# Kernel tuning notes

Measured on AMD Instinct MI355X. Metric: run time of the kernel, lower is better.

## Reference

```python
import jax, jax.numpy as jnp
import numpy as np

NEG_SLOPE = 0.2   # PyG GATConv leaky_relu default
BN_EPS = 1e-5


def setup_inputs() -> dict:
    key = jax.random.key(0)
    ks = jax.random.split(key, 6)
    B, C, N, T = 8, 128, 64, 512   # batch, in_channels, electrodes, time_steps
    H, D = 4, 32                   # heads, per-head dim; OUT = H*D = 128
    E = 256                        # knn edges (k=4 per electrode)
    OUT = H * D
    x = jax.random.normal(ks[0], (B, C, N, T), dtype=jnp.float32)
    W = jax.random.normal(ks[1], (C, H, D), dtype=jnp.float32) / np.float32(np.sqrt(C))
    att_src = jax.random.normal(ks[2], (H, D), dtype=jnp.float32) / np.float32(np.sqrt(D))
    att_dst = jax.random.normal(ks[3], (H, D), dtype=jnp.float32) / np.float32(np.sqrt(D))
    bias = jnp.zeros((OUT,), dtype=jnp.float32)
    bn_gamma = jnp.ones((OUT,), jnp.float32)
    bn_beta = jnp.zeros((OUT,), jnp.float32)
    bn_mean = jnp.zeros((OUT,), jnp.float32)   # BatchNorm running stats (eval mode)
    bn_var = jnp.ones((OUT,), jnp.float32)
    edge_index = jax.random.randint(ks[4], (2, E), 0, N, dtype=jnp.int32)
    return dict(x=x, W=W, att_src=att_src, att_dst=att_dst, bias=bias,
                bn_gamma=bn_gamma, bn_beta=bn_beta, bn_mean=bn_mean,
                bn_var=bn_var, edge_index=edge_index)


def _gat(x, W, att_src, att_dst, bias, edge_index):
    # x: [BT, N, C]; fixed graph shared across all BT slices -> fully batched
    BT, N, C = x.shape
    H, D = att_src.shape
    loops = jnp.arange(N, dtype=edge_index.dtype)
    src = jnp.concatenate([edge_index[0], loops])   # GATConv add_self_loops=True
    dst = jnp.concatenate([edge_index[1], loops])   # [E']
    h = jnp.einsum('bnc,chd->bnhd', x, W)           # [BT,N,H,D]
    a_src = jnp.einsum('bnhd,hd->bnh', h, att_src)  # [BT,N,H]
    a_dst = jnp.einsum('bnhd,hd->bnh', h, att_dst)
    scores = jax.nn.leaky_relu(a_src[:, src] + a_dst[:, dst], NEG_SLOPE)  # [BT,E',H]
    scores_e = jnp.transpose(scores, (1, 0, 2))                           # [E',BT,H]
    # segment softmax over incoming edges of each target node
    m = jax.ops.segment_max(scores_e, dst, num_segments=N)               # [N,BT,H]
    ex = jnp.exp(scores_e - m[dst])
    denom = jax.ops.segment_sum(ex, dst, num_segments=N)
    alpha = ex / denom[dst]                                               # [E',BT,H]
    msgs = alpha[..., None] * jnp.transpose(h[:, src], (1, 0, 2, 3))      # [E',BT,H,D]
    agg = jax.ops.segment_sum(msgs, dst, num_segments=N)                  # [N,BT,H,D]
    out = jnp.transpose(agg, (1, 0, 2, 3)).reshape(BT, N, H * D) + bias   # concat heads
    return out


def reference(x, W, att_src, att_dst, bias, bn_gamma, bn_beta, bn_mean, bn_var, edge_index):
    B, C, N, T = x.shape
    xt = jnp.transpose(x, (0, 3, 2, 1)).reshape(B * T, N, C)  # loop dim batched
    g = _gat(xt, W, att_src, att_dst, bias, edge_index)        # [BT,N,OUT]
    g = g.mean(axis=1)                                         # mean over nodes -> [BT,OUT]
    OUT = g.shape[-1]
    g = g.reshape(B, T, OUT).transpose(0, 2, 1)                # [B,OUT,T]
    y = (g - bn_mean[:, None]) * jax.lax.rsqrt(bn_var[:, None] + BN_EPS) \
        * bn_gamma[:, None] + bn_beta[:, None]                 # BatchNorm1d (eval)
    return y[:, :, None, :]                                    # [B,OUT,1,T]
```

## Files before the change

kernel.cpp:

```cpp
#include <hip/hip_runtime.h>
#include <math.h>

#define B_ 8
#define C_ 128
#define N_ 64
#define T_ 512
#define H_ 4
#define D_ 32
#define OUT_ 128
#define E_ 256
#define EP_ 320
#define NEG_SLOPE 0.2f
#define BN_EPS 1e-5f
#define TC 8

__global__ void setup_kernel(const float* __restrict__ W,
                             const float* __restrict__ att_src,
                             const float* __restrict__ att_dst,
                             const int* __restrict__ edge_index,
                             float* __restrict__ wa,
                             int* __restrict__ iOff_g, int* __restrict__ iSrc_g,
                             int* __restrict__ oOff_g, int* __restrict__ oDst_g) {
  __shared__ int icnt[N_], ibase[N_ + 1], ifill[N_];
  __shared__ int ocnt[N_], obase[N_ + 1], ofill[N_];
  __shared__ int esrc[EP_], edst[EP_];
  int tid = threadIdx.x;

  for (int idx = tid; idx < C_ * 8; idx += blockDim.x) {
    int c = idx >> 3, j = idx & 7, h = j & 3;
    const float* att = (j < 4) ? att_src : att_dst;
    float s = 0.f;
    for (int d = 0; d < D_; ++d)
      s += W[(c * H_ + h) * D_ + d] * att[h * D_ + d];
    wa[idx] = s;
  }
  if (tid < N_) { icnt[tid] = 0; ifill[tid] = 0; ocnt[tid] = 0; ofill[tid] = 0; }
  __syncthreads();
  for (int e = tid; e < EP_; e += blockDim.x) {
    int s, d;
    if (e < E_) { s = edge_index[e]; d = edge_index[E_ + e]; }
    else        { s = e - E_;        d = e - E_; }
    esrc[e] = s; edst[e] = d;
    atomicAdd(&icnt[d], 1);
    atomicAdd(&ocnt[s], 1);
  }
  __syncthreads();
  if (tid == 0) {
    int ai = 0, ao = 0;
    for (int n = 0; n < N_; ++n) {
      ibase[n] = ai; ai += icnt[n];
      obase[n] = ao; ao += ocnt[n];
    }
    ibase[N_] = ai; obase[N_] = ao;
  }
  __syncthreads();
  if (tid <= N_) { iOff_g[tid] = ibase[tid]; oOff_g[tid] = obase[tid]; }
  for (int e = tid; e < EP_; e += blockDim.x) {
    int s = esrc[e], d = edst[e];
    int pi = ibase[d] + atomicAdd(&ifill[d], 1);
    iSrc_g[pi] = s;
    int po = obase[s] + atomicAdd(&ofill[s], 1);
    oDst_g[po] = d;
  }
}

#define P1FMA(J, WS) \
  acc[J].x = fmaf(xv[u].x, WS, acc[J].x); \
  acc[J].y = fmaf(xv[u].y, WS, acc[J].y); \
  acc[J].z = fmaf(xv[u].z, WS, acc[J].z); \
  acc[J].w = fmaf(xv[u].w, WS, acc[J].w);

__global__ __launch_bounds__(256, 2)
void mega_kernel(const float* __restrict__ x,
                 const float* __restrict__ wa_g,
                 const float* __restrict__ W,
                 const int* __restrict__ iOff_g, const int* __restrict__ iSrc_g,
                 const int* __restrict__ oOff_g, const int* __restrict__ oDst_g,
                 const float* __restrict__ bias,
                 const float* __restrict__ bn_gamma,
                 const float* __restrict__ bn_beta,
                 const float* __restrict__ bn_mean,
                 const float* __restrict__ bn_var,
                 float* __restrict__ out) {
  __shared__ float a_l[8 * 64 * 12];
  __shared__ float4 red4[8 * 128];
  __shared__ float z_l[64 * 9 * 4];
  __shared__ float w_l[64 * 36];
  __shared__ float wal[C_ * 8];
  __shared__ int iOff[N_ + 1], oOff[N_ + 1];
  __shared__ int iSrc[EP_], oDst[EP_];

  const int tid = threadIdx.x;
  const int b = blockIdx.x & 7;
  const int tchunk = blockIdx.x >> 3;
  const int t0 = tchunk * TC;

  for (int i = tid; i < EP_; i += 256) { iSrc[i] = iSrc_g[i]; oDst[i] = oDst_g[i]; }
  if (tid <= N_) { iOff[tid] = iOff_g[tid]; oOff[tid] = oOff_g[tid]; }
  for (int i = tid; i < C_ * 8; i += 256) wal[i] = wa_g[i];
  __syncthreads();

  {
    const int cpar = __builtin_amdgcn_readfirstlane(tid >> 7);
    const int r = tid & 127;
    const int n1 = r >> 1, th = r & 1;
    const float* xp = x + ((size_t)(b * C_ + cpar) * N_ + n1) * T_ + t0 + th * 4;
    float4 acc[8];
#pragma unroll
    for (int j = 0; j < 8; ++j) { acc[j].x = 0.f; acc[j].y = 0.f; acc[j].z = 0.f; acc[j].w = 0.f; }
    for (int kb = 0; kb < 8; ++kb) {
      float4 xv[8];
#pragma unroll
      for (int u = 0; u < 8; ++u)
        xv[u] = *reinterpret_cast<const float4*>(xp + (size_t)(kb * 16 + u * 2) * (N_ * T_));
#pragma unroll
      for (int u = 0; u < 8; ++u) {
        const int c = cpar + (kb * 8 + u) * 2;
        const float4 w0 = *reinterpret_cast<const float4*>(&wal[c * 8]);
        const float4 w1 = *reinterpret_cast<const float4*>(&wal[c * 8 + 4]);
        P1FMA(0, w0.x) P1FMA(1, w0.y) P1FMA(2, w0.z) P1FMA(3, w0.w)
        P1FMA(4, w1.x) P1FMA(5, w1.y) P1FMA(6, w1.z) P1FMA(7, w1.w)
      }
    }
    if (cpar == 1) {
#pragma unroll
      for (int j = 0; j < 8; ++j) red4[j * 128 + r] = acc[j];
    }
    __syncthreads();
    if (cpar == 0) {
#pragma unroll
      for (int j = 0; j < 8; ++j) {
        float4 o = red4[j * 128 + r];
        float* ap = &a_l[j * 768 + n1 * 12 + th * 4];
        ap[0] = acc[j].x + o.x; ap[1] = acc[j].y + o.y;
        ap[2] = acc[j].z + o.z; ap[3] = acc[j].w + o.w;
      }
    }
    __syncthreads();
  }

  {
    const int t = tid & 7, grp = tid >> 3;
#pragma unroll
    for (int rep = 0; rep < 2; ++rep) {
      int nd = grp + rep * 32;
      int e0 = iOff[nd], e1 = iOff[nd + 1];
      float ad0 = a_l[4 * 768 + nd * 12 + t];
      float ad1 = a_l[5 * 768 + nd * 12 + t];
      float ad2 = a_l[6 * 768 + nd * 12 + t];
      float ad3 = a_l[7 * 768 + nd * 12 + t];
      float m0 = -1e30f, m1 = -1e30f, m2 = -1e30f, m3 = -1e30f;
      for (int e = e0; e < e1; ++e) {
        int s = iSrc[e];
        float v0 = a_l[0 * 768 + s * 12 + t] + ad0; v0 = v0 > 0.f ? v0 : NEG_SLOPE * v0;
        float v1 = a_l[1 * 768 + s * 12 + t] + ad1; v1 = v1 > 0.f ? v1 : NEG_SLOPE * v1;
        float v2 = a_l[2 * 768 + s * 12 + t] + ad2; v2 = v2 > 0.f ? v2 : NEG_SLOPE * v2;
        float v3 = a_l[3 * 768 + s * 12 + t] + ad3; v3 = v3 > 0.f ? v3 : NEG_SLOPE * v3;
        m0 = fmaxf(m0, v0); m1 = fmaxf(m1, v1);
        m2 = fmaxf(m2, v2); m3 = fmaxf(m3, v3);
      }
      float d0 = 0.f, d1 = 0.f, d2 = 0.f, d3 = 0.f;
      for (int e = e0; e < e1; ++e) {
        int s = iSrc[e];
        float v0 = a_l[0 * 768 + s * 12 + t] + ad0; v0 = v0 > 0.f ? v0 : NEG_SLOPE * v0;
        float v1 = a_l[1 * 768 + s * 12 + t] + ad1; v1 = v1 > 0.f ? v1 : NEG_SLOPE * v1;
        float v2 = a_l[2 * 768 + s * 12 + t] + ad2; v2 = v2 > 0.f ? v2 : NEG_SLOPE * v2;
        float v3 = a_l[3 * 768 + s * 12 + t] + ad3; v3 = v3 > 0.f ? v3 : NEG_SLOPE * v3;
        d0 += __expf(v0 - m0); d1 += __expf(v1 - m1);
        d2 += __expf(v2 - m2); d3 += __expf(v3 - m3);
      }
      float4 zv;
      zv.x = __expf(-m0) / (d0 * (float)N_);
      zv.y = __expf(-m1) / (d1 * (float)N_);
      zv.z = __expf(-m2) / (d2 * (float)N_);
      zv.w = __expf(-m3) / (d3 * (float)N_);
      *reinterpret_cast<float4*>(&z_l[(nd * 9 + t) * 4]) = zv;
    }
  }
  __syncthreads();

  {
    const int t = tid & 7, grp = tid >> 3;
#pragma unroll
    for (int rep = 0; rep < 2; ++rep) {
      int src = grp + rep * 32;
      int e0 = oOff[src], e1 = oOff[src + 1];
      float as0 = a_l[0 * 768 + src * 12 + t];
      float as1 = a_l[1 * 768 + src * 12 + t];
      float as2 = a_l[2 * 768 + src * 12 + t];
      float as3 = a_l[3 * 768 + src * 12 + t];
      float w0 = 0.f, w1 = 0.f, w2 = 0.f, w3 = 0.f;
      for (int e = e0; e < e1; ++e) {
        int d = oDst[e];
        float4 zv = *reinterpret_cast<const float4*>(&z_l[(d * 9 + t) * 4]);
        float v0 = as0 + a_l[4 * 768 + d * 12 + t]; v0 = v0 > 0.f ? v0 : NEG_SLOPE * v0;
        float v1 = as1 + a_l[5 * 768 + d * 12 + t]; v1 = v1 > 0.f ? v1 : NEG_SLOPE * v1;
        float v2 = as2 + a_l[6 * 768 + d * 12 + t]; v2 = v2 > 0.f ? v2 : NEG_SLOPE * v2;
        float v3 = as3 + a_l[7 * 768 + d * 12 + t]; v3 = v3 > 0.f ? v3 : NEG_SLOPE * v3;
        w0 += __expf(v0) * zv.x;
        w1 += __expf(v1) * zv.y;
        w2 += __expf(v2) * zv.z;
        w3 += __expf(v3) * zv.w;
      }
      w_l[src * 36 +  0 + t] = w0;
      w_l[src * 36 +  8 + t] = w1;
      w_l[src * 36 + 16 + t] = w2;
      w_l[src * 36 + 24 + t] = w3;
    }
  }
  __syncthreads();

  {
    const int cl = tid >> 1, g = tid & 1;
    const float* xb = x + ((size_t)(b * C_) + cl) * N_ * T_ + t0 + g * 4;
    float4 yr[4];
#pragma unroll
    for (int h = 0; h < 4; ++h) { yr[h].x = 0.f; yr[h].y = 0.f; yr[h].z = 0.f; yr[h].w = 0.f; }
    for (int nb = 0; nb < 8; ++nb) {
      float4 xv[8];
#pragma unroll
      for (int u = 0; u < 8; ++u)
        xv[u] = *reinterpret_cast<const float4*>(xb + (size_t)(nb * 8 + u) * T_);
#pragma unroll
      for (int u = 0; u < 8; ++u) {
        const int n = nb * 8 + u;
#pragma unroll
        for (int h = 0; h < 4; ++h) {
          float4 wv = *reinterpret_cast<const float4*>(&w_l[n * 36 + h * 8 + g * 4]);
          yr[h].x = fmaf(xv[u].x, wv.x, yr[h].x);
          yr[h].y = fmaf(xv[u].y, wv.y, yr[h].y);
          yr[h].z = fmaf(xv[u].z, wv.z, yr[h].z);
          yr[h].w = fmaf(xv[u].w, wv.w, yr[h].w);
        }
      }
    }
    float* y_l = a_l;
#pragma unroll
    for (int h = 0; h < 4; ++h) {
      y_l[h * 1152 + cl * 9 + g * 4 + 0] = yr[h].x;
      y_l[h * 1152 + cl * 9 + g * 4 + 1] = yr[h].y;
      y_l[h * 1152 + cl * 9 + g * 4 + 2] = yr[h].z;
      y_l[h * 1152 + cl * 9 + g * 4 + 3] = yr[h].w;
    }
  }
  __syncthreads();

  {
    const int t3 = tid & 7, g3 = tid >> 3;
    const int h = g3 >> 3, d0 = (g3 & 7) * 4;
    const float* y_l = a_l;
    float acc[4] = {0.f, 0.f, 0.f, 0.f};
#pragma unroll 4
    for (int c = 0; c < C_; ++c) {
      float yv = y_l[h * 1152 + c * 9 + t3];
      const float4 wv = *reinterpret_cast<const float4*>(
          &W[((size_t)c * H_ + h) * D_ + d0]);
      acc[0] = fmaf(yv, wv.x, acc[0]); acc[1] = fmaf(yv, wv.y, acc[1]);
      acc[2] = fmaf(yv, wv.z, acc[2]); acc[3] = fmaf(yv, wv.w, acc[3]);
    }
#pragma unroll
    for (int k = 0; k < 4; ++k) {
      int oc = h * D_ + d0 + k;
      float scale = bn_gamma[oc] * rsqrtf(bn_var[oc] + BN_EPS);
      float shift = bn_beta[oc] - bn_mean[oc] * scale;
      out[((size_t)b * OUT_ + oc) * T_ + t0 + t3] =
          (acc[k] + bias[oc]) * scale + shift;
    }
  }
}

extern "C" void kernel_launch(void* const* d_in, const int* in_sizes, int n_in,
                              void* d_out, int out_size, void* d_ws, size_t ws_size,
                              hipStream_t stream) {
  const float* x        = (const float*)d_in[0];
  const float* W        = (const float*)d_in[1];
  const float* att_src  = (const float*)d_in[2];
  const float* att_dst  = (const float*)d_in[3];
  const float* bias     = (const float*)d_in[4];
  const float* bn_gamma = (const float*)d_in[5];
  const float* bn_beta  = (const float*)d_in[6];
  const float* bn_mean  = (const float*)d_in[7];
  const float* bn_var   = (const float*)d_in[8];
  const int* edge_index = (const int*)d_in[9];
  float* out = (float*)d_out;

  char* ws = (char*)d_ws;
  float* wa   = (float*)ws;
  int* iOff_g = (int*)(ws + 4096);
  int* iSrc_g = (int*)(ws + 4608);
  int* oOff_g = (int*)(ws + 6144);
  int* oDst_g = (int*)(ws + 6656);

  setup_kernel<<<1, 256, 0, stream>>>(W, att_src, att_dst, edge_index, wa,
                                      iOff_g, iSrc_g, oOff_g, oDst_g);
  mega_kernel<<<512, 256, 0, stream>>>(x, wa, W, iOff_g, iSrc_g, oOff_g, oDst_g,
                                       bias, bn_gamma, bn_beta, bn_mean, bn_var,
                                       out);
}
```

Measured before the change: 82.49 us.

## Split fused GAT kernel into projection, aggregation and output kernels with wider time tiles

Replaces the single fused kernel with three kernels: an attention-logit projection writing to workspace, an aggregation kernel computing softmax weights and the node-weighted channel sums, and an output kernel applying W, bias and batchnorm. Time tiles widen from 8 to 32 steps so x is read in longer contiguous segments. The cost is extra launches, intermediate global round-trips, duplicated softmax work across channel-half blocks, and one 1024-thread block per CU.

```diff
diff --git a/kernel.cpp b/kernel.cpp
--- a/kernel.cpp
+++ b/kernel.cpp
@@ -12,7 +12,12 @@
 #define EP_ 320
 #define NEG_SLOPE 0.2f
 #define BN_EPS 1e-5f
-#define TC 8
+#define TCK 32
+#define NT_ (N_ * T_)
+
+#define FMA4(A, X, S) \
+  A.x = fmaf(X.x, S, A.x); A.y = fmaf(X.y, S, A.y); \
+  A.z = fmaf(X.z, S, A.z); A.w = fmaf(X.w, S, A.w);
 
 __global__ void setup_kernel(const float* __restrict__ W,
                              const float* __restrict__ att_src,
@@ -64,169 +69,208 @@
   }
 }
 
-#define P1FMA(J, WS) \
-  acc[J].x = fmaf(xv[u].x, WS, acc[J].x); \
-  acc[J].y = fmaf(xv[u].y, WS, acc[J].y); \
-  acc[J].z = fmaf(xv[u].z, WS, acc[J].z); \
-  acc[J].w = fmaf(xv[u].w, WS, acc[J].w);
-
-__global__ __launch_bounds__(256, 2)
-void mega_kernel(const float* __restrict__ x,
+__global__ __launch_bounds__(1024, 1)
+void proj_kernel(const float* __restrict__ x,
                  const float* __restrict__ wa_g,
-                 const float* __restrict__ W,
-                 const int* __restrict__ iOff_g, const int* __restrict__ iSrc_g,
-                 const int* __restrict__ oOff_g, const int* __restrict__ oDst_g,
-                 const float* __restrict__ bias,
-                 const float* __restrict__ bn_gamma,
-                 const float* __restrict__ bn_beta,
-                 const float* __restrict__ bn_mean,
-                 const float* __restrict__ bn_var,
-                 float* __restrict__ out) {
-  __shared__ float a_l[8 * 64 * 12];
-  __shared__ float4 red4[8 * 128];
-  __shared__ float z_l[64 * 9 * 4];
-  __shared__ float w_l[64 * 36];
+                 float* __restrict__ a_ws) {
   __shared__ float wal[C_ * 8];
-  __shared__ int iOff[N_ + 1], oOff[N_ + 1];
-  __shared__ int iSrc[EP_], oDst[EP_];
-
+  __shared__ float bufA[8 * 32 * 40];
+  __shared__ float bufB[8 * 32 * 40];
   const int tid = threadIdx.x;
   const int b = blockIdx.x & 7;
-  const int tchunk = blockIdx.x >> 3;
-  const int t0 = tchunk * TC;
-
-  for (int i = tid; i < EP_; i += 256) { iSrc[i] = iSrc_g[i]; oDst[i] = oDst_g[i]; }
-  if (tid <= N_) { iOff[tid] = iOff_g[tid]; oOff[tid] = oOff_g[tid]; }
-  for (int i = tid; i < C_ * 8; i += 256) wal[i] = wa_g[i];
-  __syncthreads();
-
+  const int rest = blockIdx.x >> 3;
+  const int tc = rest >> 1, nh = rest & 1;
+  const int t0 = tc * TCK;
+
+  for (int i = tid; i < C_ * 8; i += 1024) wal[i] = wa_g[i];
+  __syncthreads();
+
+  const int cs = tid >> 8;
+  const int nl = (tid >> 3) & 31;
+  const int q  = tid & 7;
+  const int n  = nh * 32 + nl;
+  const float* xp = x + ((size_t)(b * C_ + cs * 32) * N_ + n) * T_ + t0 + q * 4;
+
+  float4 acc[8];
+#pragma unroll
+  for (int j = 0; j < 8; ++j) { acc[j].x = 0.f; acc[j].y = 0.f; acc[j].z = 0.f; acc[j].w = 0.f; }
+  for (int kb = 0; kb < 4; ++kb) {
+    float4 xv[8];
+#pragma unroll
+    for (int u = 0; u < 8; ++u)
+      xv[u] = *reinterpret_cast<const float4*>(xp + (size_t)(kb * 8 + u) * NT_);
+#pragma unroll
+    for (int u = 0; u < 8; ++u) {
+      const int c = cs * 32 + kb * 8 + u;
+      const float4 w0 = *reinterpret_cast<const float4*>(&wal[c * 8]);
+      const float4 w1 = *reinterpret_cast<const float4*>(&wal[c * 8 + 4]);
+      FMA4(acc[0], xv[u], w0.x) FMA4(acc[1], xv[u], w0.y)
+      FMA4(acc[2], xv[u], w0.z) FMA4(acc[3], xv[u], w0.w)
+      FMA4(acc[4], xv[u], w1.x) FMA4(acc[5], xv[u], w1.y)
+      FMA4(acc[6], xv[u], w1.z) FMA4(acc[7], xv[u], w1.w)
+    }
+  }
+  if (cs == 1) {
+#pragma unroll
+    for (int j = 0; j < 8; ++j)
+      *reinterpret_cast<float4*>(&bufA[j * 1280 + nl * 40 + q * 4]) = acc[j];
+  } else if (cs == 3) {
+#pragma unroll
+    for (int j = 0; j < 8; ++j)
+      *reinterpret_cast<float4*>(&bufB[j * 1280 + nl * 40 + q * 4]) = acc[j];
+  }
+  __syncthreads();
+  if (cs == 0) {
+#pragma unroll
+    for (int j = 0; j < 8; ++j) {
+      float4 o = *reinterpret_cast<const float4*>(&bufA[j * 1280 + nl * 40 + q * 4]);
+      acc[j].x += o.x; acc[j].y += o.y; acc[j].z += o.z; acc[j].w += o.w;
+    }
+  } else if (cs == 2) {
+#pragma unroll
+    for (int j = 0; j < 8; ++j) {
+      float4 o = *reinterpret_cast<const float4*>(&bufB[j * 1280 + nl * 40 + q * 4]);
+      acc[j].x += o.x; acc[j].y += o.y; acc[j].z += o.z; acc[j].w += o.w;
+      *reinterpret_cast<float4*>(&bufB[j * 1280 + nl * 40 + q * 4]) = acc[j];
+    }
+  }
+  __syncthreads();
+  if (cs == 0) {
+#pragma unroll
+    for (int j = 0; j < 8; ++j) {
+      float4 o = *reinterpret_cast<const float4*>(&bufB[j * 1280 + nl * 40 + q * 4]);
+      acc[j].x += o.x; acc[j].y += o.y; acc[j].z += o.z; acc[j].w += o.w;
+      *reinterpret_cast<float4*>(
+          &a_ws[((((size_t)(b * 16 + tc)) * 64 + n) * 8 + j) * 32 + q * 4]) = acc[j];
+    }
+  }
+}
+
+__global__ __launch_bounds__(1024, 1)
+void agg_kernel(const float* __restrict__ x,
+                const float* __restrict__ a_ws,
+                const int* __restrict__ iOff_g, const int* __restrict__ iSrc_g,
+                const int* __restrict__ oOff_g, const int* __restrict__ oDst_g,
+                float* __restrict__ y_ws) {
+  __shared__ float a_l[64 * 8 * 36];
+  __shared__ float z_l[64 * 4 * 36];
+  __shared__ float w_l[64 * 4 * 36];
+  __shared__ int iSrc[EP_], oDst[EP_];
+  __shared__ int iOff[N_ + 1], oOff[N_ + 1];
+  const int tid = threadIdx.x;
+  const int b = blockIdx.x & 7;
+  const int rest = blockIdx.x >> 3;
+  const int tc = rest >> 1, ch = rest & 1;
+  const int t0 = tc * TCK;
+
+  if (tid < EP_) { iSrc[tid] = iSrc_g[tid]; oDst[tid] = oDst_g[tid]; }
+  else if (tid < EP_ + N_ + 1) {
+    int i = tid - EP_;
+    iOff[i] = iOff_g[i]; oOff[i] = oOff_g[i];
+  }
   {
-    const int cpar = __builtin_amdgcn_readfirstlane(tid >> 7);
-    const int r = tid & 127;
-    const int n1 = r >> 1, th = r & 1;
-    const float* xp = x + ((size_t)(b * C_ + cpar) * N_ + n1) * T_ + t0 + th * 4;
-    float4 acc[8];
-#pragma unroll
-    for (int j = 0; j < 8; ++j) { acc[j].x = 0.f; acc[j].y = 0.f; acc[j].z = 0.f; acc[j].w = 0.f; }
-    for (int kb = 0; kb < 8; ++kb) {
-      float4 xv[8];
-#pragma unroll
-      for (int u = 0; u < 8; ++u)
-        xv[u] = *reinterpret_cast<const float4*>(xp + (size_t)(kb * 16 + u * 2) * (N_ * T_));
-#pragma unroll
-      for (int u = 0; u < 8; ++u) {
-        const int c = cpar + (kb * 8 + u) * 2;
-        const float4 w0 = *reinterpret_cast<const float4*>(&wal[c * 8]);
-        const float4 w1 = *reinterpret_cast<const float4*>(&wal[c * 8 + 4]);
-        P1FMA(0, w0.x) P1FMA(1, w0.y) P1FMA(2, w0.z) P1FMA(3, w0.w)
-        P1FMA(4, w1.x) P1FMA(5, w1.y) P1FMA(6, w1.z) P1FMA(7, w1.w)
-      }
-    }
-    if (cpar == 1) {
-#pragma unroll
-      for (int j = 0; j < 8; ++j) red4[j * 128 + r] = acc[j];
-    }
-    __syncthreads();
-    if (cpar == 0) {
-#pragma unroll
-      for (int j = 0; j < 8; ++j) {
-        float4 o = red4[j * 128 + r];
-        float* ap = &a_l[j * 768 + n1 * 12 + th * 4];
-        ap[0] = acc[j].x + o.x; ap[1] = acc[j].y + o.y;
-        ap[2] = acc[j].z + o.z; ap[3] = acc[j].w + o.w;
-      }
-    }
-    __syncthreads();
-  }
+    const float4* src = reinterpret_cast<const float4*>(
+        a_ws + (size_t)(b * 16 + tc) * (64 * 8 * 32));
+#pragma unroll
+    for (int f = 0; f < 4; ++f) {
+      int g = f * 1024 + tid;
+      int nn = g >> 6, j = (g >> 3) & 7, q = g & 7;
+      *reinterpret_cast<float4*>(&a_l[nn * 288 + j * 36 + q * 4]) = src[g];
+    }
+  }
+  __syncthreads();
 
   {
-    const int t = tid & 7, grp = tid >> 3;
+    const int t = tid & 31, g = tid >> 5;
 #pragma unroll
     for (int rep = 0; rep < 2; ++rep) {
-      int nd = grp + rep * 32;
+      int nd = g + rep * 32;
       int e0 = iOff[nd], e1 = iOff[nd + 1];
-      float ad0 = a_l[4 * 768 + nd * 12 + t];
-      float ad1 = a_l[5 * 768 + nd * 12 + t];
-      float ad2 = a_l[6 * 768 + nd * 12 + t];
-      float ad3 = a_l[7 * 768 + nd * 12 + t];
+      float ad0 = a_l[nd * 288 + 4 * 36 + t];
+      float ad1 = a_l[nd * 288 + 5 * 36 + t];
+      float ad2 = a_l[nd * 288 + 6 * 36 + t];
+      float ad3 = a_l[nd * 288 + 7 * 36 + t];
       float m0 = -1e30f, m1 = -1e30f, m2 = -1e30f, m3 = -1e30f;
       for (int e = e0; e < e1; ++e) {
         int s = iSrc[e];
-        float v0 = a_l[0 * 768 + s * 12 + t] + ad0; v0 = v0 > 0.f ? v0 : NEG_SLOPE * v0;
-        float v1 = a_l[1 * 768 + s * 12 + t] + ad1; v1 = v1 > 0.f ? v1 : NEG_SLOPE * v1;
-        float v2 = a_l[2 * 768 + s * 12 + t] + ad2; v2 = v2 > 0.f ? v2 : NEG_SLOPE * v2;
-        float v3 = a_l[3 * 768 + s * 12 + t] + ad3; v3 = v3 > 0.f ? v3 : NEG_SLOPE * v3;
+        float v0 = a_l[s * 288 + 0 * 36 + t] + ad0; v0 = v0 > 0.f ? v0 : NEG_SLOPE * v0;
+        float v1 = a_l[s * 288 + 1 * 36 + t] + ad1; v1 = v1 > 0.f ? v1 : NEG_SLOPE * v1;
+        float v2 = a_l[s * 288 + 2 * 36 + t] + ad2; v2 = v2 > 0.f ? v2 : NEG_SLOPE * v2;
+        float v3 = a_l[s * 288 + 3 * 36 + t] + ad3; v3 = v3 > 0.f ? v3 : NEG_SLOPE * v3;
         m0 = fmaxf(m0, v0); m1 = fmaxf(m1, v1);
         m2 = fmaxf(m2, v2); m3 = fmaxf(m3, v3);
       }
       float d0 = 0.f, d1 = 0.f, d2 = 0.f, d3 = 0.f;
       for (int e = e0; e < e1; ++e) {
         int s = iSrc[e];
-        float v0 = a_l[0 * 768 + s * 12 + t] + ad0; v0 = v0 > 0.f ? v0 : NEG_SLOPE * v0;
-        float v1 = a_l[1 * 768 + s * 12 + t] + ad1; v1 = v1 > 0.f ? v1 : NEG_SLOPE * v1;
-        float v2 = a_l[2 * 768 + s * 12 + t] + ad2; v2 = v2 > 0.f ? v2 : NEG_SLOPE * v2;
-        float v3 = a_l[3 * 768 + s * 12 + t] + ad3; v3 = v3 > 0.f ? v3 : NEG_SLOPE * v3;
+        float v0 = a_l[s * 288 + 0 * 36 + t] + ad0; v0 = v0 > 0.f ? v0 : NEG_SLOPE * v0;
+        float v1 = a_l[s * 288 + 1 * 36 + t] + ad1; v1 = v1 > 0.f ? v1 : NEG_SLOPE * v1;
+        float v2 = a_l[s * 288 + 2 * 36 + t] + ad2; v2 = v2 > 0.f ? v2 : NEG_SLOPE * v2;
+        float v3 = a_l[s * 288 + 3 * 36 + t] + ad3; v3 = v3 > 0.f ? v3 : NEG_SLOPE * v3;
         d0 += __expf(v0 - m0); d1 += __expf(v1 - m1);
         d2 += __expf(v2 - m2); d3 += __expf(v3 - m3);
       }
-      float4 zv;
-      zv.x = __expf(-m0) / (d0 * (float)N_);
-      zv.y = __expf(-m1) / (d1 * (float)N_);
-      zv.z = __expf(-m2) / (d2 * (float)N_);
-      zv.w = __expf(-m3) / (d3 * (float)N_);
-      *reinterpret_cast<float4*>(&z_l[(nd * 9 + t) * 4]) = zv;
+      z_l[nd * 144 + 0 * 36 + t] = __expf(-m0) / (d0 * (float)N_);
+      z_l[nd * 144 + 1 * 36 + t] = __expf(-m1) / (d1 * (float)N_);
+      z_l[nd * 144 + 2 * 36 + t] = __expf(-m2) / (d2 * (float)N_);
+      z_l[nd * 144 + 3 * 36 + t] = __expf(-m3) / (d3 * (float)N_);
     }
   }
   __syncthreads();
 
   {
-    const int t = tid & 7, grp = tid >> 3;
+    const int t = tid & 31, g = tid >> 5;
 #pragma unroll
     for (int rep = 0; rep < 2; ++rep) {
-      int src = grp + rep * 32;
+      int src = g + rep * 32;
       int e0 = oOff[src], e1 = oOff[src + 1];
-      float as0 = a_l[0 * 768 + src * 12 + t];
-      float as1 = a_l[1 * 768 + src * 12 + t];
-      float as2 = a_l[2 * 768 + src * 12 + t];
-      float as3 = a_l[3 * 768 + src * 12 + t];
+      float as0 = a_l[src * 288 + 0 * 36 + t];
+      float as1 = a_l[src * 288 + 1 * 36 + t];
+      float as2 = a_l[src * 288 + 2 * 36 + t];
+      float as3 = a_l[src * 288 + 3 * 36 + t];
       float w0 = 0.f, w1 = 0.f, w2 = 0.f, w3 = 0.f;
       for (int e = e0; e < e1; ++e) {
         int d = oDst[e];
-        float4 zv = *reinterpret_cast<const float4*>(&z_l[(d * 9 + t) * 4]);
-        float v0 = as0 + a_l[4 * 768 + d * 12 + t]; v0 = v0 > 0.f ? v0 : NEG_SLOPE * v0;
-        float v1 = as1 + a_l[5 * 768 + d * 12 + t]; v1 = v1 > 0.f ? v1 : NEG_SLOPE * v1;
-        float v2 = as2 + a_l[6 * 768 + d * 12 + t]; v2 = v2 > 0.f ? v2 : NEG_SLOPE * v2;
-        float v3 = as3 + a_l[7 * 768 + d * 12 + t]; v3 = v3 > 0.f ? v3 : NEG_SLOPE * v3;
-        w0 += __expf(v0) * zv.x;
-        w1 += __expf(v1) * zv.y;
-        w2 += __expf(v2) * zv.z;
-        w3 += __expf(v3) * zv.w;
-      }
-      w_l[src * 36 +  0 + t] = w0;
-      w_l[src * 36 +  8 + t] = w1;
-      w_l[src * 36 + 16 + t] = w2;
-      w_l[src * 36 + 24 + t] = w3;
+        float z0 = z_l[d * 144 + 0 * 36 + t];
+        float z1 = z_l[d * 144 + 1 * 36 + t];
+        float z2 = z_l[d * 144 + 2 * 36 + t];
+        float z3 = z_l[d * 144 + 3 * 36 + t];
+        float v0 = as0 + a_l[d * 288 + 4 * 36 + t]; v0 = v0 > 0.f ? v0 : NEG_SLOPE * v0;
+        float v1 = as1 + a_l[d * 288 + 5 * 36 + t]; v1 = v1 > 0.f ? v1 : NEG_SLOPE * v1;
+        float v2 = as2 + a_l[d * 288 + 6 * 36 + t]; v2 = v2 > 0.f ? v2 : NEG_SLOPE * v2;
+        float v3 = as3 + a_l[d * 288 + 7 * 36 + t]; v3 = v3 > 0.f ? v3 : NEG_SLOPE * v3;
+        w0 += __expf(v0) * z0;
+        w1 += __expf(v1) * z1;
+        w2 += __expf(v2) * z2;
+        w3 += __expf(v3) * z3;
+      }
+      w_l[src * 144 + 0 * 36 + t] = w0;
+      w_l[src * 144 + 1 * 36 + t] = w1;
+      w_l[src * 144 + 2 * 36 + t] = w2;
+      w_l[src * 144 + 3 * 36 + t] = w3;
     }
   }
   __syncthreads();
 
   {
-    const int cl = tid >> 1, g = tid & 1;
-    const float* xb = x + ((size_t)(b * C_) + cl) * N_ * T_ + t0 + g * 4;
+    const int c  = tid >> 4;
+    const int q  = (tid >> 1) & 7;
+    const int ns = tid & 1;
+    const float* xp = x + ((size_t)(b * C_ + ch * 64 + c) * N_ + ns * 32) * T_ + t0 + q * 4;
     float4 yr[4];
 #pragma unroll
     for (int h = 0; h < 4; ++h) { yr[h].x = 0.f; yr[h].y = 0.f; yr[h].z = 0.f; yr[h].w = 0.f; }
-    for (int nb = 0; nb < 8; ++nb) {
+    for (int ib = 0; ib < 4; ++ib) {
       float4 xv[8];
 #pragma unroll
       for (int u = 0; u < 8; ++u)
-        xv[u] = *reinterpret_cast<const float4*>(xb + (size_t)(nb * 8 + u) * T_);
+        xv[u] = *reinterpret_cast<const float4*>(xp + (size_t)(ib * 8 + u) * T_);
 #pragma unroll
       for (int u = 0; u < 8; ++u) {
-        const int n = nb * 8 + u;
+        const int n = ns * 32 + ib * 8 + u;
 #pragma unroll
         for (int h = 0; h < 4; ++h) {
-          float4 wv = *reinterpret_cast<const float4*>(&w_l[n * 36 + h * 8 + g * 4]);
+          float4 wv = *reinterpret_cast<const float4*>(&w_l[n * 144 + h * 36 + q * 4]);
           yr[h].x = fmaf(xv[u].x, wv.x, yr[h].x);
           yr[h].y = fmaf(xv[u].y, wv.y, yr[h].y);
           yr[h].z = fmaf(xv[u].z, wv.z, yr[h].z);
@@ -234,38 +278,64 @@
         }
       }
     }
-    float* y_l = a_l;
-#pragma unroll
-    for (int h = 0; h < 4; ++h) {
-      y_l[h * 1152 + cl * 9 + g * 4 + 0] = yr[h].x;
-      y_l[h * 1152 + cl * 9 + g * 4 + 1] = yr[h].y;
-      y_l[h * 1152 + cl * 9 + g * 4 + 2] = yr[h].z;
-      y_l[h * 1152 + cl * 9 + g * 4 + 3] = yr[h].w;
-    }
-  }
-  __syncthreads();
-
-  {
-    const int t3 = tid & 7, g3 = tid >> 3;
-    const int h = g3 >> 3, d0 = (g3 & 7) * 4;
-    const float* y_l = a_l;
-    float acc[4] = {0.f, 0.f, 0.f, 0.f};
+    float* scr = a_l;
+    if (ns == 1) {
+#pragma unroll
+      for (int h = 0; h < 4; ++h)
+        *reinterpret_cast<float4*>(&scr[c * 144 + h * 36 + q * 4]) = yr[h];
+    }
+    __syncthreads();
+    if (ns == 0) {
+#pragma unroll
+      for (int h = 0; h < 4; ++h) {
+        float4 o = *reinterpret_cast<const float4*>(&scr[c * 144 + h * 36 + q * 4]);
+        yr[h].x += o.x; yr[h].y += o.y; yr[h].z += o.z; yr[h].w += o.w;
+        *reinterpret_cast<float4*>(
+            &y_ws[(((size_t)(b * 4 + h) * 128) + ch * 64 + c) * 512 + t0 + q * 4]) = yr[h];
+      }
+    }
+  }
+}
+
+__global__ void out_kernel(const float* __restrict__ y_ws,
+                           const float* __restrict__ W,
+                           const float* __restrict__ bias,
+                           const float* __restrict__ bn_gamma,
+                           const float* __restrict__ bn_beta,
+                           const float* __restrict__ bn_mean,
+                           const float* __restrict__ bn_var,
+                           float* __restrict__ out) {
+  __shared__ float wl[C_ * D_];
+  int blk = blockIdx.x;
+  int b = blk & 7;
+  int h = (blk >> 3) & 3;
+  int tcb = blk >> 5;
+  int tid = threadIdx.x;
+  int t = tcb * 64 + (tid & 63);
+  int d0 = (tid >> 6) * 8;
+  for (int i = tid; i < C_ * D_; i += 256) {
+    int c = i >> 5, d = i & 31;
+    wl[i] = W[((size_t)c * H_ + h) * D_ + d];
+  }
+  __syncthreads();
+  float acc[8] = {0.f, 0.f, 0.f, 0.f, 0.f, 0.f, 0.f, 0.f};
+  const float* yp = y_ws + ((size_t)b * H_ + h) * C_ * T_ + t;
 #pragma unroll 4
-    for (int c = 0; c < C_; ++c) {
-      float yv = y_l[h * 1152 + c * 9 + t3];
-      const float4 wv = *reinterpret_cast<const float4*>(
-          &W[((size_t)c * H_ + h) * D_ + d0]);
-      acc[0] = fmaf(yv, wv.x, acc[0]); acc[1] = fmaf(yv, wv.y, acc[1]);
-      acc[2] = fmaf(yv, wv.z, acc[2]); acc[3] = fmaf(yv, wv.w, acc[3]);
-    }
-#pragma unroll
-    for (int k = 0; k < 4; ++k) {
-      int oc = h * D_ + d0 + k;
-      float scale = bn_gamma[oc] * rsqrtf(bn_var[oc] + BN_EPS);
-      float shift = bn_beta[oc] - bn_mean[oc] * scale;
-      out[((size_t)b * OUT_ + oc) * T_ + t0 + t3] =
-          (acc[k] + bias[oc]) * scale + shift;
-    }
+  for (int c = 0; c < C_; ++c) {
+    float yv = yp[(size_t)c * T_];
+    const float4 w0 = *reinterpret_cast<const float4*>(&wl[c * D_ + d0]);
+    const float4 w1 = *reinterpret_cast<const float4*>(&wl[c * D_ + d0 + 4]);
+    acc[0] = fmaf(yv, w0.x, acc[0]); acc[1] = fmaf(yv, w0.y, acc[1]);
+    acc[2] = fmaf(yv, w0.z, acc[2]); acc[3] = fmaf(yv, w0.w, acc[3]);
+    acc[4] = fmaf(yv, w1.x, acc[4]); acc[5] = fmaf(yv, w1.y, acc[5]);
+    acc[6] = fmaf(yv, w1.z, acc[6]); acc[7] = fmaf(yv, w1.w, acc[7]);
+  }
+#pragma unroll
+  for (int k = 0; k < 8; ++k) {
+    int oc = h * D_ + d0 + k;
+    float scale = bn_gamma[oc] * rsqrtf(bn_var[oc] + BN_EPS);
+    float shift = bn_beta[oc] - bn_mean[oc] * scale;
+    out[((size_t)b * OUT_ + oc) * T_ + t] = (acc[k] + bias[oc]) * scale + shift;
   }
 }
 
@@ -290,10 +360,14 @@
   int* iSrc_g = (int*)(ws + 4608);
   int* oOff_g = (int*)(ws + 6144);
   int* oDst_g = (int*)(ws + 6656);
+  float* a_ws = (float*)(ws + 16384);
+  float* y_ws = (float*)(ws + 16384 + (size_t)8 * 1024 * 1024);
 
   setup_kernel<<<1, 256, 0, stream>>>(W, att_src, att_dst, edge_index, wa,
                                       iOff_g, iSrc_g, oOff_g, oDst_g);
-  mega_kernel<<<512, 256, 0, stream>>>(x, wa, W, iOff_g, iSrc_g, oOff_g, oDst_g,
-                                       bias, bn_gamma, bn_beta, bn_mean, bn_var,
-                                       out);
-}
+  proj_kernel<<<256, 1024, 0, stream>>>(x, wa, a_ws);
+  agg_kernel<<<256, 1024, 0, stream>>>(x, a_ws, iOff_g, iSrc_g, oOff_g, oDst_g,
+                                       y_ws);
+  out_kernel<<<256, 256, 0, stream>>>(y_ws, W, bias, bn_gamma, bn_beta,
+                                      bn_mean, bn_var, out);
+}
```

New measurement: 91.91 us. 1.11x slower.
